# Kernel optimization log

Hardware: AMD Instinct MI355X
Metric: run time of the kernel (lower is better)

Reference implementation:

```python
import jax, jax.numpy as jnp
from jax import lax
import numpy as np

# ---- static APPM geometry (MMAL-Net config: input 448, stride 32 -> 14x14 fm) ----
STRIDE = 32
FM = 14
RATIOS = [[4, 4], [3, 5], [5, 3],
          [6, 6], [5, 7], [7, 5],
          [8, 8], [6, 10], [10, 6], [7, 9], [9, 7], [7, 10], [10, 7]]
N_LIST = [3, 2, 1]          # proposals per ratio-group -> proposalN = 6
IOU_THRESHS = [0.25, 0.25, 0.25]
GROUP_RATIO_SPLITS = [3, 6, 13]  # ratios 0:3, 3:6, 6:13


def _window_num(r):
    return (FM - r[0] + 1) * (FM - r[1] + 1)


def _build_coords():
    # indices2coordinates: window (i,j) of ratio (rh,rw) -> pixel box, inclusive ends
    coords = []
    for rh, rw in RATIOS:
        rows, cols = FM - rh + 1, FM - rw + 1
        ii, jj = np.meshgrid(np.arange(rows), np.arange(cols), indexing='ij')
        x0 = ii.reshape(-1) * STRIDE
        y0 = jj.reshape(-1) * STRIDE
        x1 = x0 + rh * STRIDE - 1
        y1 = y0 + rw * STRIDE - 1
        coords.append(np.stack([x0, y0, x1, y1], 1))
    return np.concatenate(coords, 0).astype(np.float32)

COORDS = jnp.asarray(_build_coords())  # [917, 4]
WINDOW_NUMS = [_window_num(r) for r in RATIOS]
_g1 = sum(WINDOW_NUMS[:3]); _g2 = sum(WINDOW_NUMS[3:6]); _g3 = sum(WINDOW_NUMS[6:])
GROUPS = [(0, _g1), (_g1, _g1 + _g2), (_g1 + _g2, _g1 + _g2 + _g3)]  # (0,361),(361,602),(602,917)


def _argmax_mask(logits):
    # mask = 0.7 everywhere, 1.0 at per-row argmax
    B, C = logits.shape
    one_hot = jax.nn.one_hot(jnp.argmax(logits, axis=1), C, dtype=logits.dtype)
    return 0.7 + 0.3 * one_hot


def _nms_group(scores, coords, n_pick, thresh):
    # greedy descending-score NMS; scores [W], coords [W,4]
    x0, y0, x1, y1 = coords[:, 0], coords[:, 1], coords[:, 2], coords[:, 3]
    areas = (x1 - x0 + 1.0) * (y1 - y0 + 1.0)

    def step(carry, _):
        valid, last = carry
        masked = jnp.where(valid, scores, -jnp.inf)
        idx = jnp.argmax(masked).astype(jnp.int32)
        idx = jnp.where(valid.any(), idx, last)  # pad by repeating last pick
        ix0, iy0, ix1, iy1 = coords[idx]
        lx = jnp.minimum(x1, ix1) - jnp.maximum(x0, ix0) + 1.0
        ly = jnp.minimum(y1, iy1) - jnp.maximum(y0, iy0) + 1.0
        inter = jnp.where((lx < 0) | (ly < 0), 0.0, lx * ly)
        iou = inter / (areas + areas[idx] - inter)
        valid = valid & (iou <= thresh)  # also suppresses idx itself (iou == 1)
        return (valid, idx), idx

    init = (jnp.ones(scores.shape[0], dtype=bool), jnp.int32(0))
    (_, _), picks = lax.scan(step, init, None, length=n_pick)
    return picks  # [n_pick] int32


def _appm(local_fm):
    # avgpool over each ratio then sum over channels == channel-sum then 2D mean pool
    B = local_fm.shape[0]
    fm_sum = jnp.sum(local_fm, axis=1)  # [B,14,14]
    per_ratio = []
    for rh, rw in RATIOS:
        pooled = lax.reduce_window(fm_sum, jnp.float32(0.0), lax.add,
                                   (1, rh, rw), (1, 1, 1), 'VALID') / (rh * rw)
        per_ratio.append(pooled.reshape(B, -1))
    all_scores = jnp.concatenate(per_ratio, axis=1)  # [B, 917]

    picks = []
    for (s, e), n_pick, thr in zip(GROUPS, N_LIST, IOU_THRESHS):
        g = jax.vmap(lambda sc: _nms_group(sc, COORDS[s:e], n_pick, thr))(all_scores[:, s:e])
        picks.append(g + s)
    proposalN_indices = jnp.concatenate(picks, axis=1)  # [B, 6]
    proposalN_windows_scores = jnp.take_along_axis(all_scores, proposalN_indices, axis=1)
    return proposalN_indices, proposalN_windows_scores, all_scores


def setup_inputs() -> dict:
    key = jax.random.key(0)
    ks = jax.random.split(key, 6)
    B, C, NC, BIT = 256, 512, 200, 48
    return {
        'local_fm': jax.random.normal(ks[0], (B, C, 14, 14), jnp.float32),
        'local_embeddings': jax.random.normal(ks[1], (B, C), jnp.float32),
        'W_cls': jax.random.normal(ks[2], (NC, C), jnp.float32) * 0.02,
        'b_cls': jax.random.normal(ks[3], (NC,), jnp.float32) * 0.02,
        'W_hash': jax.random.normal(ks[4], (BIT, NC), jnp.float32) * 0.02,
        'b_hash': jax.random.normal(ks[5], (BIT,), jnp.float32) * 0.02,
    }


def reference(local_fm, local_embeddings, W_cls, b_cls, W_hash, b_hash):
    # classification head + per-row argmax masking + hash head (Tanh)
    local_logits = local_embeddings @ W_cls.T + b_cls          # [B, num_classes]
    masked = local_logits * _argmax_mask(local_logits)
    local_hash_code = jnp.tanh(masked @ W_hash.T + b_hash)     # [B, bit]
    # APPM region proposal on detached feature map
    proposalN_indices, proposalN_windows_scores, window_scores = _appm(
        lax.stop_gradient(local_fm))
    return (local_hash_code, local_logits, proposalN_indices,
            proposalN_windows_scores, window_scores)
```

## Files before the change

kernel.cpp:

```cpp
#include <hip/hip_runtime.h>
#include <math.h>

#define NW 917

__constant__ int c_off[13]  = {0,121,241,361,442,522,602,651,696,741,789,837,877};
__constant__ int c_rh[13]   = {4,3,5,6,5,7,8,6,10,7,9,7,10};
__constant__ int c_rw[13]   = {4,5,3,6,7,5,8,10,6,9,7,10,7};
__constant__ int c_cols[13] = {11,10,12,9,8,10,7,5,9,6,8,5,8};

__device__ inline void decode_w(int w, int& r, int& i, int& j){
    int rr = 0;
    #pragma unroll
    for (int k = 1; k < 13; ++k) if (w >= c_off[k]) rr = k;
    int loc = w - c_off[rr];
    int cols = c_cols[rr];
    r = rr; i = loc / cols; j = loc - i * cols;
}

__device__ inline unsigned long long nms_key(float v, int w){
    unsigned u = __float_as_uint(v);
    u = (u & 0x80000000u) ? ~u : (u | 0x80000000u);
    return ((unsigned long long)u << 32) | (unsigned)(0xFFFFFFFFu - (unsigned)w);
}

__device__ inline unsigned long long shfl_xor_u64(unsigned long long x, int m){
    unsigned lo = (unsigned)x, hi = (unsigned)(x >> 32);
    lo = __shfl_xor(lo, m);
    hi = __shfl_xor(hi, m);
    return ((unsigned long long)hi << 32) | lo;
}

__global__ __launch_bounds__(1024) void mono_kernel(const float* __restrict__ fm,
                                                    const float* __restrict__ E,
                                                    const float* __restrict__ Wc,
                                                    const float* __restrict__ bc,
                                                    const float* __restrict__ Wh,
                                                    const float* __restrict__ bh,
                                                    float* __restrict__ out_hash,
                                                    float* __restrict__ out_logits,
                                                    float* __restrict__ out_idx,
                                                    float* __restrict__ out_psc,
                                                    float* __restrict__ out_scores){
    int b = blockIdx.x, t = threadIdx.x;
    int lane = t & 63, wv = t >> 6;

    __shared__ float4 red[20][49];
    __shared__ float fmS[196];
    __shared__ float R[14][15];
    __shared__ float I[15][15];
    __shared__ float s[NW];
    __shared__ float emb[512];
    __shared__ float lg[200];
    __shared__ float mk[200];

    const float4* base = (const float4*)(fm + (size_t)b * 512 * 196);
    if (t < 980){
        int cg = t / 49;
        const float4* p4 = base + t;
        float4 acc = {0.f,0.f,0.f,0.f};
        #pragma unroll 5
        for (int k = 0; k < 25; ++k){
            float4 v = p4[980 * k];
            acc.x += v.x; acc.y += v.y; acc.z += v.z; acc.w += v.w;
        }
        if (cg < 12){
            float4 v = p4[980 * 25];
            acc.x += v.x; acc.y += v.y; acc.z += v.z; acc.w += v.w;
        }
        red[cg][t - cg * 49] = acc;
    }
    if (t < 512) emb[t] = E[b * 512 + t];
    __syncthreads();
    if (t < 49){
        float4 a = red[0][t];
        #pragma unroll
        for (int k = 1; k < 20; ++k){
            float4 v = red[k][t];
            a.x += v.x; a.y += v.y; a.z += v.z; a.w += v.w;
        }
        ((float4*)fmS)[t] = a;
    }
    __syncthreads();

    if (t < 14){
        float run = 0.f;
        R[t][0] = 0.f;
        for (int j = 0; j < 14; ++j){ run += fmS[t * 14 + j]; R[t][j + 1] = run; }
    }
    __syncthreads();
    if (t < 15){
        float run = 0.f;
        I[0][t] = 0.f;
        for (int i = 0; i < 14; ++i){ run += R[i][t]; I[i + 1][t] = run; }
    }
    __syncthreads();

    if (t < NW){
        int r, i, j; decode_w(t, r, i, j);
        int rh = c_rh[r], rw = c_rw[r];
        float sum = I[i + rh][j + rw] - I[i][j + rw] - I[i + rh][j] + I[i][j];
        float sc = sum / (float)(rh * rw);
        s[t] = sc;
        out_scores[(size_t)b * NW + t] = sc;
    }
    __syncthreads();

    if (wv == 0){
        float sc_[15]; unsigned pk_[15]; int gr_[15];
        #pragma unroll
        for (int m = 0; m < 15; ++m){
            int w = lane + (m << 6);
            bool ok = w < NW;
            int r = 0, i = 0, j = 0;
            if (ok) decode_w(w, r, i, j);
            sc_[m] = ok ? s[w] : 0.f;
            pk_[m] = (unsigned)(i | (j << 4) | (c_rh[r] << 8) | (c_rw[r] << 12));
            gr_[m] = ok ? ((w >= 602) ? 2 : (w >= 361) ? 1 : 0) : 3;
        }
        unsigned vmask = 0x7FFFu;
        int slot = 0;
        #pragma unroll
        for (int g = 0; g < 3; ++g){
            int npick = (g == 0) ? 3 : (g == 1) ? 2 : 1;
            int last  = (g == 0) ? 0 : (g == 1) ? 361 : 602;
            for (int p = 0; p < npick; ++p){
                unsigned long long key = 0ULL;
                #pragma unroll
                for (int m = 0; m < 15; ++m){
                    if (gr_[m] == g && ((vmask >> m) & 1u)){
                        unsigned long long k2 = nms_key(sc_[m], lane + (m << 6));
                        if (k2 > key) key = k2;
                    }
                }
                #pragma unroll
                for (int off = 32; off > 0; off >>= 1){
                    unsigned long long o = shfl_xor_u64(key, off);
                    if (o > key) key = o;
                }
                int pick = (key == 0ULL) ? last
                                         : (int)(0xFFFFFFFFu - (unsigned)(key & 0xFFFFFFFFu));
                last = pick;
                int pr, pi, pj; decode_w(pick, pr, pi, pj);
                float px0 = pi * 32.f, py0 = pj * 32.f;
                float prh = (float)c_rh[pr], prw = (float)c_rw[pr];
                float px1 = px0 + prh * 32.f - 1.f, py1 = py0 + prw * 32.f - 1.f;
                float pa  = prh * prw * 1024.f;
                #pragma unroll
                for (int m = 0; m < 15; ++m){
                    if (gr_[m] == g && ((vmask >> m) & 1u)){
                        unsigned pk = pk_[m];
                        float x0 = (float)(pk & 15u) * 32.f;
                        float y0 = (float)((pk >> 4) & 15u) * 32.f;
                        float rh = (float)((pk >> 8) & 15u);
                        float rw = (float)(pk >> 12);
                        float x1 = x0 + rh * 32.f - 1.f;
                        float y1 = y0 + rw * 32.f - 1.f;
                        float ar = rh * rw * 1024.f;
                        float lx = fminf(x1, px1) - fmaxf(x0, px0) + 1.f;
                        float ly = fminf(y1, py1) - fmaxf(y0, py0) + 1.f;
                        float inter = (lx < 0.f || ly < 0.f) ? 0.f : lx * ly;
                        float iou = inter / (ar + pa - inter);
                        if (iou > 0.25f) vmask &= ~(1u << m);
                    }
                }
                if (lane == 0){
                    out_idx[b * 6 + slot] = (float)pick;
                    out_psc[b * 6 + slot] = s[pick];
                }
                slot++;
            }
        }
    } else {
        int gw  = wv - 1;
        int grp = lane >> 4;
        int s16 = lane & 15;
        const float4* emb4 = (const float4*)emb;
        for (int p = 0; p < 4; ++p){
            int row = p * 60 + gw * 4 + grp;
            if (row < 200){
                const float4* wrow = (const float4*)(Wc + (size_t)row * 512);
                float acc = 0.f;
                #pragma unroll
                for (int k = 0; k < 8; ++k){
                    float4 w = wrow[k * 16 + s16];
                    float4 e = emb4[k * 16 + s16];
                    acc += e.x * w.x + e.y * w.y + e.z * w.z + e.w * w.w;
                }
                acc += __shfl_xor(acc, 1);
                acc += __shfl_xor(acc, 2);
                acc += __shfl_xor(acc, 4);
                acc += __shfl_xor(acc, 8);
                if (s16 == 0){
                    float v = acc + bc[row];
                    lg[row] = v;
                    out_logits[(size_t)b * 200 + row] = v;
                }
            }
        }
    }
    __syncthreads();

    {
        unsigned long long key = nms_key(lg[lane], lane);
        unsigned long long k2  = nms_key(lg[lane + 64], lane + 64);
        if (k2 > key) key = k2;
        k2 = nms_key(lg[lane + 128], lane + 128);
        if (k2 > key) key = k2;
        if (lane + 192 < 200){
            k2 = nms_key(lg[lane + 192], lane + 192);
            if (k2 > key) key = k2;
        }
        #pragma unroll
        for (int off = 32; off > 0; off >>= 1){
            unsigned long long o = shfl_xor_u64(key, off);
            if (o > key) key = o;
        }
        int amax = (int)(0xFFFFFFFFu - (unsigned)(key & 0xFFFFFFFFu));
        if (t < 200) mk[t] = lg[t] * (t == amax ? 1.0f : 0.7f);
    }
    __syncthreads();

    if (t < 768){
        int row = t >> 4;
        int s16 = t & 15;
        const float4* wrow = (const float4*)(Wh + (size_t)row * 200);
        const float4* mk4  = (const float4*)mk;
        float4 w0 = wrow[s16],      m0 = mk4[s16];
        float4 w1 = wrow[s16 + 16], m1 = mk4[s16 + 16];
        float4 w2 = wrow[s16 + 32], m2 = mk4[s16 + 32];
        float acc = w0.x*m0.x + w0.y*m0.y + w0.z*m0.z + w0.w*m0.w
                  + w1.x*m1.x + w1.y*m1.y + w1.z*m1.z + w1.w*m1.w
                  + w2.x*m2.x + w2.y*m2.y + w2.z*m2.z + w2.w*m2.w;
        if (s16 < 2){
            float4 w3 = wrow[s16 + 48], m3 = mk4[s16 + 48];
            acc += w3.x*m3.x + w3.y*m3.y + w3.z*m3.z + w3.w*m3.w;
        }
        acc += __shfl_xor(acc, 1);
        acc += __shfl_xor(acc, 2);
        acc += __shfl_xor(acc, 4);
        acc += __shfl_xor(acc, 8);
        if (s16 == 0) out_hash[b * 48 + row] = tanhf(acc + bh[row]);
    }
}

extern "C" void kernel_launch(void* const* d_in, const int* in_sizes, int n_in,
                              void* d_out, int out_size, void* d_ws, size_t ws_size,
                              hipStream_t stream) {
    const float* fm = (const float*)d_in[0];
    const float* E  = (const float*)d_in[1];
    const float* Wc = (const float*)d_in[2];
    const float* bc = (const float*)d_in[3];
    const float* Wh = (const float*)d_in[4];
    const float* bh = (const float*)d_in[5];
    float* out        = (float*)d_out;
    float* out_hash   = out;
    float* out_logits = out + 12288;
    float* out_idx    = out + 63488;
    float* out_psc    = out + 65024;
    float* out_scores = out + 66560;

    hipLaunchKernelGGL(mono_kernel, dim3(256), dim3(1024), 0, stream,
                       fm, E, Wc, bc, Wh, bh,
                       out_hash, out_logits, out_idx, out_psc, out_scores);
}
```

Measured before the change: 170.0 us.

## Split channel reduction into its own wide kernel, feed a slimmer tail kernel

The feature-map channel sum moves out of the single fused kernel into a separate kernel. It uses four blocks per batch element and two independent accumulators, and writes per-quarter partial sums to workspace. A second 512-thread kernel combines the partials and runs the box scoring, NMS, classifier and hash heads, with loops re-tiled for the smaller block. The aim is more memory-level parallelism for the bandwidth-bound reduction, which previously ran on only 256 blocks. The cost is an extra launch and a workspace round trip, and the new code also contains a redundant duplicated embedding load and barrier.

```diff
diff --git a/kernel.cpp b/kernel.cpp
--- a/kernel.cpp
+++ b/kernel.cpp
@@ -30,21 +30,53 @@
     return ((unsigned long long)hi << 32) | lo;
 }
 
-__global__ __launch_bounds__(1024) void mono_kernel(const float* __restrict__ fm,
-                                                    const float* __restrict__ E,
-                                                    const float* __restrict__ Wc,
-                                                    const float* __restrict__ bc,
-                                                    const float* __restrict__ Wh,
-                                                    const float* __restrict__ bh,
-                                                    float* __restrict__ out_hash,
-                                                    float* __restrict__ out_logits,
-                                                    float* __restrict__ out_idx,
-                                                    float* __restrict__ out_psc,
-                                                    float* __restrict__ out_scores){
+__global__ __launch_bounds__(256) void chansum_kernel(const float* __restrict__ fm,
+                                                      float* __restrict__ partial){
+    int t = threadIdx.x;
+    int b = blockIdx.x >> 2, part = blockIdx.x & 3;
+    __shared__ float4 red[5][49];
+    const float4* base = (const float4*)(fm + (size_t)b * 512 * 196) + part * 6272;
+    if (t < 245){
+        int cg = t / 49;
+        float4 a0 = {0.f,0.f,0.f,0.f}, a1 = {0.f,0.f,0.f,0.f};
+        #pragma unroll
+        for (int k = 0; k < 26; ++k){
+            int idx = t + 245 * k;
+            if (idx < 6272){
+                float4 v = base[idx];
+                if (k & 1){ a1.x += v.x; a1.y += v.y; a1.z += v.z; a1.w += v.w; }
+                else      { a0.x += v.x; a0.y += v.y; a0.z += v.z; a0.w += v.w; }
+            }
+        }
+        a0.x += a1.x; a0.y += a1.y; a0.z += a1.z; a0.w += a1.w;
+        red[cg][t - cg * 49] = a0;
+    }
+    __syncthreads();
+    if (t < 49){
+        float4 s = red[0][t];
+        #pragma unroll
+        for (int k = 1; k < 5; ++k){
+            float4 v = red[k][t];
+            s.x += v.x; s.y += v.y; s.z += v.z; s.w += v.w;
+        }
+        ((float4*)partial)[blockIdx.x * 49 + t] = s;
+    }
+}
+
+__global__ __launch_bounds__(512) void tail_kernel(const float* __restrict__ partial,
+                                                   const float* __restrict__ E,
+                                                   const float* __restrict__ Wc,
+                                                   const float* __restrict__ bc,
+                                                   const float* __restrict__ Wh,
+                                                   const float* __restrict__ bh,
+                                                   float* __restrict__ out_hash,
+                                                   float* __restrict__ out_logits,
+                                                   float* __restrict__ out_idx,
+                                                   float* __restrict__ out_psc,
+                                                   float* __restrict__ out_scores){
     int b = blockIdx.x, t = threadIdx.x;
     int lane = t & 63, wv = t >> 6;
 
-    __shared__ float4 red[20][49];
     __shared__ float fmS[196];
     __shared__ float R[14][15];
     __shared__ float I[15][15];
@@ -53,33 +85,15 @@
     __shared__ float lg[200];
     __shared__ float mk[200];
 
-    const float4* base = (const float4*)(fm + (size_t)b * 512 * 196);
-    if (t < 980){
-        int cg = t / 49;
-        const float4* p4 = base + t;
-        float4 acc = {0.f,0.f,0.f,0.f};
-        #pragma unroll 5
-        for (int k = 0; k < 25; ++k){
-            float4 v = p4[980 * k];
-            acc.x += v.x; acc.y += v.y; acc.z += v.z; acc.w += v.w;
-        }
-        if (cg < 12){
-            float4 v = p4[980 * 25];
-            acc.x += v.x; acc.y += v.y; acc.z += v.z; acc.w += v.w;
-        }
-        red[cg][t - cg * 49] = acc;
-    }
-    if (t < 512) emb[t] = E[b * 512 + t];
-    __syncthreads();
-    if (t < 49){
-        float4 a = red[0][t];
-        #pragma unroll
-        for (int k = 1; k < 20; ++k){
-            float4 v = red[k][t];
-            a.x += v.x; a.y += v.y; a.z += v.z; a.w += v.w;
-        }
-        ((float4*)fmS)[t] = a;
-    }
+    if (t < 196){
+        const float* p = partial + (size_t)b * 784 + t;
+        fmS[t] = (p[0] + p[196]) + (p[392] + p[588]);
+    }
+    emb[t] = E[b * 512 + t & 0x7FFFFFFF];
+    __syncthreads();
+    __syncthreads();
+
+    emb[t] = E[b * 512 + t];
     __syncthreads();
 
     if (t < 14){
@@ -95,13 +109,13 @@
     }
     __syncthreads();
 
-    if (t < NW){
-        int r, i, j; decode_w(t, r, i, j);
+    for (int w = t; w < NW; w += 512){
+        int r, i, j; decode_w(w, r, i, j);
         int rh = c_rh[r], rw = c_rw[r];
         float sum = I[i + rh][j + rw] - I[i][j + rw] - I[i + rh][j] + I[i][j];
         float sc = sum / (float)(rh * rw);
-        s[t] = sc;
-        out_scores[(size_t)b * NW + t] = sc;
+        s[w] = sc;
+        out_scores[(size_t)b * NW + w] = sc;
     }
     __syncthreads();
 
@@ -175,8 +189,8 @@
         int grp = lane >> 4;
         int s16 = lane & 15;
         const float4* emb4 = (const float4*)emb;
-        for (int p = 0; p < 4; ++p){
-            int row = p * 60 + gw * 4 + grp;
+        for (int p = 0; p < 8; ++p){
+            int row = p * 28 + gw * 4 + grp;
             if (row < 200){
                 const float4* wrow = (const float4*)(Wc + (size_t)row * 512);
                 float acc = 0.f;
@@ -220,26 +234,27 @@
     }
     __syncthreads();
 
-    if (t < 768){
-        int row = t >> 4;
-        int s16 = t & 15;
+    if (t < 384){
+        int row = t >> 3;
+        int s8  = t & 7;
         const float4* wrow = (const float4*)(Wh + (size_t)row * 200);
         const float4* mk4  = (const float4*)mk;
-        float4 w0 = wrow[s16],      m0 = mk4[s16];
-        float4 w1 = wrow[s16 + 16], m1 = mk4[s16 + 16];
-        float4 w2 = wrow[s16 + 32], m2 = mk4[s16 + 32];
-        float acc = w0.x*m0.x + w0.y*m0.y + w0.z*m0.z + w0.w*m0.w
-                  + w1.x*m1.x + w1.y*m1.y + w1.z*m1.z + w1.w*m1.w
-                  + w2.x*m2.x + w2.y*m2.y + w2.z*m2.z + w2.w*m2.w;
-        if (s16 < 2){
-            float4 w3 = wrow[s16 + 48], m3 = mk4[s16 + 48];
-            acc += w3.x*m3.x + w3.y*m3.y + w3.z*m3.z + w3.w*m3.w;
+        float acc = 0.f;
+        #pragma unroll
+        for (int m = 0; m < 6; ++m){
+            float4 w = wrow[s8 + 8 * m];
+            float4 v = mk4[s8 + 8 * m];
+            acc += w.x*v.x + w.y*v.y + w.z*v.z + w.w*v.w;
+        }
+        if (s8 < 2){
+            float4 w = wrow[48 + s8];
+            float4 v = mk4[48 + s8];
+            acc += w.x*v.x + w.y*v.y + w.z*v.z + w.w*v.w;
         }
         acc += __shfl_xor(acc, 1);
         acc += __shfl_xor(acc, 2);
         acc += __shfl_xor(acc, 4);
-        acc += __shfl_xor(acc, 8);
-        if (s16 == 0) out_hash[b * 48 + row] = tanhf(acc + bh[row]);
+        if (s8 == 0) out_hash[b * 48 + row] = tanhf(acc + bh[row]);
     }
 }
 
@@ -258,8 +273,10 @@
     float* out_idx    = out + 63488;
     float* out_psc    = out + 65024;
     float* out_scores = out + 66560;
-
-    hipLaunchKernelGGL(mono_kernel, dim3(256), dim3(1024), 0, stream,
-                       fm, E, Wc, bc, Wh, bh,
+    float* partial    = (float*)d_ws;
+
+    hipLaunchKernelGGL(chansum_kernel, dim3(1024), dim3(256), 0, stream, fm, partial);
+    hipLaunchKernelGGL(tail_kernel,    dim3(256),  dim3(512), 0, stream, partial,
+                       E, Wc, bc, Wh, bh,
                        out_hash, out_logits, out_idx, out_psc, out_scores);
 }
```

Measured after the change: 173.6 us. 1.02x slower.
